# Performance work log

Measured on AMD Instinct MI355X. Metric: run time of the kernel, lower is better.

## Reference

```python
import jax, jax.numpy as jnp
import numpy as np

B, SZ_C, S, D_KV, H_DIM = 2048, 8, 32, 32, 512
NEG = B // 4  # batchsize > 64 branch
TEMP = 0.5
EPS = 1e-8
BN_EPS = 1e-5


def setup_inputs() -> dict:
    key = jax.random.key(0)
    ks = jax.random.split(key, 8)
    x = jax.random.normal(ks[0], (B, SZ_C, S, D_KV), dtype=jnp.float32)
    W1 = jax.random.normal(ks[1], (H_DIM, D_KV), dtype=jnp.float32) * 0.05
    b1 = jnp.zeros((H_DIM,), jnp.float32)
    gamma = jnp.ones((H_DIM,), jnp.float32)
    beta = jnp.zeros((H_DIM,), jnp.float32)
    W2 = jax.random.normal(ks[2], (D_KV, H_DIM), dtype=jnp.float32) * 0.05
    b2 = jnp.zeros((D_KV,), jnp.float32)
    fcW = jax.random.normal(ks[3], (32, S * D_KV), dtype=jnp.float32) * 0.03
    fcb = jnp.zeros((32,), jnp.float32)
    # negatives: raw draws in [0, B-1); shifted past the self index inside reference
    neg_idx = jax.random.randint(ks[4], (B, NEG), 0, B - 1, dtype=jnp.int32)
    return {"x": x, "W1": W1, "b1": b1, "gamma": gamma, "beta": beta,
            "W2": W2, "b2": b2, "fcW": fcW, "fcb": fcb, "neg_idx": neg_idx}


def reference(x, W1, b1, gamma, beta, W2, b2, fcW, fcb, neg_idx):
    # per-channel MLP with training-mode BatchNorm (stats over the B*S rows of each channel)
    xc = jnp.transpose(x, (1, 0, 2, 3)).reshape(SZ_C, B * S, D_KV)   # [C, N, d_kv]
    h = jnp.einsum('cnd,hd->cnh', xc, W1) + b1                        # [C, N, h]
    mu = jnp.mean(h, axis=1, keepdims=True)
    var = jnp.mean((h - mu) ** 2, axis=1, keepdims=True)              # biased, as BN
    h = jax.nn.relu((h - mu) * jax.lax.rsqrt(var + BN_EPS) * gamma + beta)
    y = jnp.einsum('cnh,dh->cnd', h, W2) + b2                         # [C, N, d_kv]
    y = y.reshape(SZ_C, B, S * D_KV)                                  # raw flatten == torch views
    Zc = jnp.einsum('cbf,of->cbo', y, fcW) + fcb                      # [C, B, 32]
    Z = jnp.transpose(Zc, (1, 0, 2))                                  # [B, C, 32]

    Zn = Z / jnp.clip(jnp.linalg.norm(Z, axis=-1, keepdims=True), EPS, None)

    # shift raw draws in [0, B-1) past i -> uniform over indices != i
    idx = neg_idx + (neg_idx >= jnp.arange(B, dtype=neg_idx.dtype)[:, None]).astype(neg_idx.dtype)
    neg = Zn[idx]                                                     # [B, NEG, C, 32]
    neg_sim = jnp.einsum('bcd,bncd->bn', Zn, neg) / SZ_C              # mean over channels

    # mean pairwise cosine similarity across channels (j < k)
    G = jnp.einsum('bjd,bkd->bjk', Zn, Zn)                            # [B, C, C]
    mask = jnp.triu(jnp.ones((SZ_C, SZ_C), bool), 1)
    num_comb = SZ_C * (SZ_C - 1) // 2
    pos_sim = jnp.where(mask, G, 0.0).sum(axis=(1, 2)) / num_comb     # [B]

    l = jnp.exp(pos_sim / TEMP) / jnp.sum(jnp.exp(neg_sim / TEMP), axis=1)  # [B]
    Z_out = jnp.mean(Z, axis=1)                                       # [B, 32]
    return Z_out, l
```

## Files before the change

kernel.cpp:

```cpp
#include <hip/hip_runtime.h>
#include <hip/hip_bf16.h>
#include <math.h>

#define NB 2048
#define NC 8
#define NNEG 512

typedef __attribute__((ext_vector_type(8))) short bf16x8;
typedef __attribute__((ext_vector_type(4))) float f32x4;
typedef __attribute__((ext_vector_type(16))) float f32x16;

static __device__ __forceinline__ unsigned short f2b(float f) {
  __hip_bfloat16 h = __float2bfloat16(f);
  return *reinterpret_cast<unsigned short*>(&h);
}
static __device__ __forceinline__ unsigned int pack_rn(float a, float b) {
  unsigned int ua = __float_as_uint(a) + 0x8000u;
  unsigned int ub = __float_as_uint(b) + 0x8000u;
  return __builtin_amdgcn_perm(ub, ua, 0x07060302u);
}
#define MF16(a, b, c) __builtin_amdgcn_mfma_f32_16x16x32_bf16((a), (b), (c), 0, 0, 0)

#define WS_SSUM   0
#define WS_SPROD  256
#define WS_B1EFF  8448
#define WS_Z      12544
#define WS_POS    536832
#define WS_W1B    538880
#define WS_W2B    604416
#define WS_FCWB   612608
#define WS_ZNB    628992

__global__ __launch_bounds__(256) void k_stats(const float* __restrict__ x,
                        float* __restrict__ Ssum, float* __restrict__ Sprod) {
  int c = blockIdx.y;
  int t = threadIdx.x;
  int w = t >> 6, l = t & 63;
  int col = l & 31, half = l >> 5;
  f32x16 acc;
  #pragma unroll
  for (int r = 0; r < 16; ++r) acc[r] = 0.f;
  float ssum = 0.f;
  #pragma unroll 2
  for (int i = 0; i < 8; ++i) {
    int chunk = blockIdx.x * 32 + i * 4 + w;
    int b = chunk >> 1;
    int sb = (chunk & 1) * 16 + half * 8;
    const float* base = x + ((size_t)(b * NC + c)) * 1024 + sb * 32 + col;
    float v0 = base[0],   v1 = base[32],  v2 = base[64],  v3 = base[96];
    float v4 = base[128], v5 = base[160], v6 = base[192], v7 = base[224];
    ssum += ((v0 + v1) + (v2 + v3)) + ((v4 + v5) + (v6 + v7));
    uint4 fq;
    fq.x = pack_rn(v0, v1); fq.y = pack_rn(v2, v3);
    fq.z = pack_rn(v4, v5); fq.w = pack_rn(v6, v7);
    bf16x8 f = __builtin_bit_cast(bf16x8, fq);
    acc = __builtin_amdgcn_mfma_f32_32x32x16_bf16(f, f, acc, 0, 0, 0);
  }
  __shared__ float pr[4][1024];
  __shared__ float sred[4][32];
  #pragma unroll
  for (int r = 0; r < 16; ++r) {
    int row = (r & 3) + 8 * (r >> 2) + 4 * half;
    pr[w][row * 32 + col] = acc[r];
  }
  float sv = ssum + __shfl_xor(ssum, 32);
  if (l < 32) sred[w][l] = sv;
  __syncthreads();
  #pragma unroll
  for (int p = 0; p < 4; ++p) {
    int cell = t + p * 256;
    atomicAdd(&Sprod[c * 1024 + cell],
              (pr[0][cell] + pr[1][cell]) + (pr[2][cell] + pr[3][cell]));
  }
  if (t < 32)
    atomicAdd(&Ssum[c * 32 + t],
              (sred[0][t] + sred[1][t]) + (sred[2][t] + sred[3][t]));
}

__global__ void k_foldcvt(const float* __restrict__ W1, const float* __restrict__ b1,
                       const float* __restrict__ gamma, const float* __restrict__ beta,
                       const float* __restrict__ Ssum, const float* __restrict__ Sprod,
                       const float* __restrict__ W2, const float* __restrict__ fcW,
                       unsigned short* __restrict__ W1B, float* __restrict__ b1eff,
                       unsigned short* __restrict__ W2B, unsigned short* __restrict__ fcWB) {
  if (blockIdx.x >= 16) {
    int j = (blockIdx.x - 16) * 256 + threadIdx.x;
    if (j < 8192)
      ((unsigned int*)W2B)[j] = pack_rn(W2[2 * j], W2[2 * j + 1]);
    ((unsigned int*)fcWB)[j] = pack_rn(fcW[2 * j], fcW[2 * j + 1]);
    return;
  }
  int g = blockIdx.x * 256 + threadIdx.x;
  int c = g >> 9, h = g & 511;
  const float invN = 1.0f / (float)(NB * 32);
  float w[32];
  #pragma unroll
  for (int d = 0; d < 32; ++d) w[d] = W1[h * 32 + d];
  const float* M = Sprod + c * 1024;
  float q = 0.f;
  for (int j = 0; j < 32; ++j) {
    float v = 0.f;
    #pragma unroll
    for (int i2 = 0; i2 < 32; ++i2) v = fmaf(w[i2], M[i2 * 32 + j], v);
    q = fmaf(v, w[j], q);
  }
  float wmu = 0.f;
  #pragma unroll
  for (int d = 0; d < 32; ++d) wmu = fmaf(w[d], Ssum[c * 32 + d] * invN, wmu);
  float bb = b1[h];
  float mean = wmu + bb;
  float e2 = q * invN + 2.f * bb * wmu + bb * bb;
  float var = e2 - mean * mean;
  float alpha = gamma[h] * rsqrtf(var + 1e-5f);
  unsigned int* W1Bu = (unsigned int*)&W1B[((size_t)c * 512 + h) * 32];
  #pragma unroll
  for (int d = 0; d < 16; ++d)
    W1Bu[d] = pack_rn(w[2 * d] * alpha, w[2 * d + 1] * alpha);
  b1eff[c * 512 + h] = (bb - mean) * alpha + beta[h];
}

__global__ __launch_bounds__(256, 2) void k_main(
    const float* __restrict__ x, const unsigned short* __restrict__ W1B,
    const float* __restrict__ b1eff, const unsigned short* __restrict__ W2B,
    const float* __restrict__ b2, const unsigned short* __restrict__ fcWB,
    const float* __restrict__ fcb, float* __restrict__ Z) {
  int c = blockIdx.y;
  int bt0 = blockIdx.x * 4;
  int t = threadIdx.x;
  int w = t >> 6, l = t & 63;
  int lr = l & 15, lg = l >> 4;

  __shared__ unsigned int rbuf[4][64][20];
  __shared__ float zred[2][8][32];

  const unsigned short* W1c = W1B + (size_t)c * 512 * 32;
  const float* b1e = b1eff + c * 512;
  unsigned int* rbw = &rbuf[w][0][0];

  bf16x8 wfR[2];   f32x4 biasR[2];   bf16x8 w2fR[2];   bf16x8 hfreg[4];
  bf16x8 xf[4], xfN[4];

#define LOADX(dst, bti) \
  _Pragma("unroll") for (int sb = 0; sb < 4; ++sb) { \
    int bl = 2 * w + (sb >> 1); \
    int s = (sb & 1) * 16 + lr; \
    const float* src = x + (((size_t)((bti) * 8 + bl) * NC + c) * 32 + s) * 32 + lg * 8; \
    float4 v0 = ((const float4*)src)[0]; \
    float4 v1 = ((const float4*)src)[1]; \
    uint4 fq; \
    fq.x = pack_rn(v0.x, v0.y); fq.y = pack_rn(v0.z, v0.w); \
    fq.z = pack_rn(v1.x, v1.y); fq.w = pack_rn(v1.z, v1.w); \
    dst[sb] = __builtin_bit_cast(bf16x8, fq); \
  }

#define LDWF0() { \
    wfR[0]  = *(const bf16x8*)&W1c[(size_t)lr * 32 + lg * 8]; \
    wfR[1]  = *(const bf16x8*)&W1c[(size_t)(16 + lr) * 32 + lg * 8]; \
    biasR[0] = *(const f32x4*)(b1e + lg * 4); \
    biasR[1] = *(const f32x4*)(b1e + 16 + lg * 4); }

#define GEMM1(dfr) \
  _Pragma("unroll") for (int hb = 0; hb < 2; ++hb) \
  _Pragma("unroll") for (int sb = 0; sb < 4; ++sb) \
    dfr[hb][sb] = MF16(wfR[hb], xf[sb], biasR[hb]);

#define GEMM2() \
  _Pragma("unroll") for (int mb = 0; mb < 4; ++mb) { \
    yacc[mb][0] = MF16(w2fR[0], hfreg[mb], yacc[mb][0]); \
    yacc[mb][1] = MF16(w2fR[1], hfreg[mb], yacc[mb][1]); \
  }

#define PACKWRITE(dfr) \
  _Pragma("unroll") for (int hb = 0; hb < 2; ++hb) \
  _Pragma("unroll") for (int sb = 0; sb < 4; ++sb) { \
    uint2 pk; \
    pk.x = pack_rn(fmaxf(dfr[hb][sb][0], 0.f), fmaxf(dfr[hb][sb][1], 0.f)); \
    pk.y = pack_rn(fmaxf(dfr[hb][sb][2], 0.f), fmaxf(dfr[hb][sb][3], 0.f)); \
    *(uint2*)&rbw[(sb * 16 + lr) * 20 + hb * 8 + lg * 2] = pk; \
  }

#define LOADW(ch) { \
    if ((ch) < 15) { \
      int h1 = ((ch) + 1) * 32; \
      wfR[0]  = *(const bf16x8*)&W1c[(size_t)(h1 + lr) * 32 + lg * 8]; \
      wfR[1]  = *(const bf16x8*)&W1c[(size_t)(h1 + 16 + lr) * 32 + lg * 8]; \
      biasR[0] = *(const f32x4*)(b1e + h1 + lg * 4); \
      biasR[1] = *(const f32x4*)(b1e + h1 + 16 + lg * 4); \
    } \
    w2fR[0] = *(const bf16x8*)&W2B[(size_t)lr * 512 + (ch) * 32 + lg * 8]; \
    w2fR[1] = *(const bf16x8*)&W2B[(size_t)(16 + lr) * 512 + (ch) * 32 + lg * 8]; \
  }

#define READH() \
  _Pragma("unroll") for (int mb = 0; mb < 4; ++mb) \
    hfreg[mb] = *(const bf16x8*)&rbw[(mb * 16 + lr) * 20 + lg * 4];

  LOADX(xf, bt0);
  LDWF0();

  for (int tt = 0; tt < 4; ++tt) {
    int bt = bt0 + tt;

    f32x4 yacc[4][2];
    #pragma unroll
    for (int db = 0; db < 2; ++db) {
      f32x4 bv = *((const f32x4*)(b2 + db * 16 + lg * 4));
      #pragma unroll
      for (int mb = 0; mb < 4; ++mb) yacc[mb][db] = bv;
    }

    {
      f32x4 dfr[2][4];
      GEMM1(dfr);
      PACKWRITE(dfr);
      LOADW(0);
      READH();
    }
    #pragma unroll 3
    for (int ch = 1; ch < 16; ++ch) {
      f32x4 dfr[2][4];
      GEMM1(dfr);
      GEMM2();
      PACKWRITE(dfr);
      LOADW(ch);
      READH();
    }
    GEMM2();

    if (tt < 3) LOADX(xfN, bt + 1);
    LDWF0();

    #pragma unroll
    for (int mb = 0; mb < 4; ++mb) {
      #pragma unroll
      for (int db = 0; db < 2; ++db) {
        uint2 pk;
        pk.x = pack_rn(yacc[mb][db][0], yacc[mb][db][1]);
        pk.y = pack_rn(yacc[mb][db][2], yacc[mb][db][3]);
        *(uint2*)&rbw[(mb * 16 + lr) * 20 + db * 8 + lg * 2] = pk;
      }
    }
    __syncthreads();

    {
      int nt = w & 1, kh = w >> 1;
      int arow = (lr < 8) ? lr : 7;
      const unsigned int* ybase = &rbuf[arow >> 1][(arow & 1) * 32][0];
      f32x4 zacc = {0.f, 0.f, 0.f, 0.f};
      #pragma unroll
      for (int ks = 0; ks < 16; ++ks) {
        int s = kh * 16 + ks;
        uint4 av = *(const uint4*)&ybase[s * 20 + lg * 4];
        bf16x8 afc = __builtin_bit_cast(bf16x8, av);
        bf16x8 bfc = *(const bf16x8*)&fcWB[(size_t)(nt * 16 + lr) * 1024 + s * 32 + lg * 8];
        zacc = MF16(afc, bfc, zacc);
      }
      if (lg < 2) {
        #pragma unroll
        for (int r = 0; r < 4; ++r) zred[kh][lg * 4 + r][nt * 16 + lr] = zacc[r];
      }
    }
    __syncthreads();
    {
      int bloc = t >> 5, o = t & 31;
      Z[((size_t)(bt * 8 + bloc) * NC + c) * 32 + o] =
          zred[0][bloc][o] + zred[1][bloc][o] + fcb[o];
    }
    if (tt < 3) {
      #pragma unroll
      for (int sb = 0; sb < 4; ++sb) xf[sb] = xfN[sb];
    }
  }
#undef LOADX
#undef LDWF0
#undef GEMM1
#undef GEMM2
#undef PACKWRITE
#undef LOADW
#undef READH
}

__global__ void k_znorm(const float* __restrict__ Z, unsigned short* __restrict__ Znb,
                        float* __restrict__ possim, float* __restrict__ out) {
  int b = blockIdx.x;
  int t = threadIdx.x;
  float v = Z[(size_t)b * 256 + t];
  float n2 = v * v;
  #pragma unroll
  for (int m = 16; m >= 1; m >>= 1) n2 += __shfl_xor(n2, m, 64);
  float nrm = fmaxf(sqrtf(n2), 1e-8f);
  float zn = v / nrm;
  Znb[(size_t)b * 256 + t] = f2b(zn);
  __shared__ float sz[256];
  __shared__ float szn[256];
  sz[t] = v; szn[t] = zn;
  __syncthreads();
  if (t < 32) {
    float s = 0.f;
    #pragma unroll
    for (int cc = 0; cc < 8; ++cc) s += sz[cc * 32 + t];
    out[(size_t)b * 32 + t] = s * 0.125f;
    float sd = 0.f, t1 = 0.f;
    #pragma unroll
    for (int cc = 0; cc < 8; ++cc) {
      float z2 = szn[cc * 32 + t];
      sd += z2; t1 = fmaf(z2, z2, t1);
    }
    float t2 = sd * sd;
    #pragma unroll
    for (int m = 16; m >= 1; m >>= 1) {
      t2 += __shfl_xor(t2, m, 64);
      t1 += __shfl_xor(t1, m, 64);
    }
    if (t == 0) possim[b] = (t2 - t1) * 0.5f / 28.0f;
  }
}

__global__ __launch_bounds__(256) void k_negsim(
    const unsigned short* __restrict__ Znb, const int* __restrict__ neg_idx,
    const float* __restrict__ possim, float* __restrict__ lout) {
  int b = blockIdx.x;
  int t = threadIdx.x;
  int w = t >> 6, l = t & 63;
  int lr = l & 15, lg = l >> 4;
  __shared__ uint4 selfv[32];
  __shared__ float rs[4];
  if (t < 32) selfv[t] = ((const uint4*)(Znb + (size_t)b * 256))[t];
  __syncthreads();
  const unsigned short* selfp = (const unsigned short*)selfv;
  const f32x4 fzero = {0.f, 0.f, 0.f, 0.f};
  float esum = 0.f;
  #pragma unroll 2
  for (int mb = 0; mb < 8; ++mb) {
    int m0 = w * 128 + mb * 16;
    int raw = neg_idx[(size_t)b * NNEG + m0 + lr];
    int j = raw + (raw >= b ? 1 : 0);
    const unsigned short* rp = Znb + (size_t)j * 256;
    f32x4 acc = fzero;
    #pragma unroll
    for (int ks = 0; ks < 8; ++ks) {
      bf16x8 af = *(const bf16x8*)(rp + ks * 32 + lg * 8);
      bf16x8 bf = *(const bf16x8*)(selfp + ks * 32 + lg * 8);
      acc = MF16(af, bf, acc);
    }
    if (lr == 0) {
      esum += expf(acc[0] * 0.25f) + expf(acc[1] * 0.25f)
            + expf(acc[2] * 0.25f) + expf(acc[3] * 0.25f);
    }
  }
  #pragma unroll
  for (int m = 32; m >= 1; m >>= 1) esum += __shfl_xor(esum, m, 64);
  if (l == 0) rs[w] = esum;
  __syncthreads();
  if (t == 0) {
    float tot = rs[0] + rs[1] + rs[2] + rs[3];
    lout[b] = expf(possim[b] * 2.0f) / tot;
  }
}

extern "C" void kernel_launch(void* const* d_in, const int* in_sizes, int n_in,
                              void* d_out, int out_size, void* d_ws, size_t ws_size,
                              hipStream_t stream) {
  const float* x     = (const float*)d_in[0];
  const float* W1    = (const float*)d_in[1];
  const float* b1    = (const float*)d_in[2];
  const float* gamma = (const float*)d_in[3];
  const float* beta  = (const float*)d_in[4];
  const float* W2    = (const float*)d_in[5];
  const float* b2    = (const float*)d_in[6];
  const float* fcW   = (const float*)d_in[7];
  const float* fcb   = (const float*)d_in[8];
  const int*   nidx  = (const int*)d_in[9];
  float* ws = (float*)d_ws;
  float* Ssum   = ws + WS_SSUM;
  float* Sprod  = ws + WS_SPROD;
  float* b1eff  = ws + WS_B1EFF;
  float* Z      = ws + WS_Z;
  float* possim = ws + WS_POS;
  unsigned short* W1Bp  = (unsigned short*)(ws + WS_W1B);
  unsigned short* W2Bp  = (unsigned short*)(ws + WS_W2B);
  unsigned short* fcWBp = (unsigned short*)(ws + WS_FCWB);
  unsigned short* Znbp  = (unsigned short*)(ws + WS_ZNB);
  float* out = (float*)d_out;

  hipMemsetAsync(ws, 0, (256 + 8192) * sizeof(float), stream);
  k_stats<<<dim3(128, 8), 256, 0, stream>>>(x, Ssum, Sprod);
  k_foldcvt<<<80, 256, 0, stream>>>(W1, b1, gamma, beta, Ssum, Sprod, W2, fcW,
                                    W1Bp, b1eff, W2Bp, fcWBp);
  k_main<<<dim3(64, 8), 256, 0, stream>>>(x, W1Bp, b1eff, W2Bp, b2, fcWBp, fcb, Z);
  k_znorm<<<NB, 256, 0, stream>>>(Z, Znbp, possim, out);
  k_negsim<<<NB, 256, 0, stream>>>(Znbp, nidx, possim, out + NB * 32);
}
```

Baseline: 176.9 us.

## Replace stats atomics with partial buffers and double-buffer the MLP hidden chunks

The stats kernel now writes per-block partial Gram and sum tiles to scratch instead of issuing global atomics. A new small reduction kernel sums them, which also drops the memset. The main kernel processes two hidden-dim chunks per iteration using A/B register sets and two LDS buffers, so GEMM1 of one chunk overlaps GEMM2 of the other. This raises register and LDS use and adds one kernel launch.

```diff
diff --git a/kernel.cpp b/kernel.cpp
--- a/kernel.cpp
+++ b/kernel.cpp
@@ -30,9 +30,10 @@
 #define WS_W2B    604416
 #define WS_FCWB   612608
 #define WS_ZNB    628992
+#define WS_SSUMP  891136
 
 __global__ __launch_bounds__(256) void k_stats(const float* __restrict__ x,
-                        float* __restrict__ Ssum, float* __restrict__ Sprod) {
+                        float* __restrict__ SsumP, float* __restrict__ SprodP) {
   int c = blockIdx.y;
   int t = threadIdx.x;
   int w = t >> 6, l = t & 63;
@@ -42,8 +43,8 @@
   for (int r = 0; r < 16; ++r) acc[r] = 0.f;
   float ssum = 0.f;
   #pragma unroll 2
-  for (int i = 0; i < 8; ++i) {
-    int chunk = blockIdx.x * 32 + i * 4 + w;
+  for (int i = 0; i < 16; ++i) {
+    int chunk = blockIdx.x * 64 + i * 4 + w;
     int b = chunk >> 1;
     int sb = (chunk & 1) * 16 + half * 8;
     const float* base = x + ((size_t)(b * NC + c)) * 1024 + sb * 32 + col;
@@ -69,12 +70,33 @@
   #pragma unroll
   for (int p = 0; p < 4; ++p) {
     int cell = t + p * 256;
-    atomicAdd(&Sprod[c * 1024 + cell],
-              (pr[0][cell] + pr[1][cell]) + (pr[2][cell] + pr[3][cell]));
+    SprodP[((size_t)(c * 64 + blockIdx.x)) * 1024 + cell] =
+        (pr[0][cell] + pr[1][cell]) + (pr[2][cell] + pr[3][cell]);
   }
   if (t < 32)
-    atomicAdd(&Ssum[c * 32 + t],
-              (sred[0][t] + sred[1][t]) + (sred[2][t] + sred[3][t]));
+    SsumP[(c * 64 + blockIdx.x) * 32 + t] =
+        (sred[0][t] + sred[1][t]) + (sred[2][t] + sred[3][t]);
+}
+
+__global__ void k_red(const float* __restrict__ SprodP, const float* __restrict__ SsumP,
+                      float* __restrict__ Sprod, float* __restrict__ Ssum) {
+  if (blockIdx.x < 32) {
+    int g = blockIdx.x * 256 + threadIdx.x;
+    int c = g >> 10, cell = g & 1023;
+    float s = 0.f;
+    #pragma unroll 8
+    for (int p = 0; p < 64; ++p)
+      s += SprodP[((size_t)(c * 64 + p)) * 1024 + cell];
+    Sprod[g] = s;
+  } else {
+    int t = threadIdx.x;
+    int c = t >> 5, d = t & 31;
+    float s = 0.f;
+    #pragma unroll 8
+    for (int p = 0; p < 64; ++p)
+      s += SsumP[(c * 64 + p) * 32 + d];
+    Ssum[t] = s;
+  }
 }
 
 __global__ void k_foldcvt(const float* __restrict__ W1, const float* __restrict__ b1,
@@ -130,14 +152,17 @@
   int w = t >> 6, l = t & 63;
   int lr = l & 15, lg = l >> 4;
 
-  __shared__ unsigned int rbuf[4][64][20];
+  __shared__ unsigned int rbuf[4][2][64][20];
   __shared__ float zred[2][8][32];
 
   const unsigned short* W1c = W1B + (size_t)c * 512 * 32;
   const float* b1e = b1eff + c * 512;
-  unsigned int* rbw = &rbuf[w][0][0];
-
-  bf16x8 wfR[2];   f32x4 biasR[2];   bf16x8 w2fR[2];   bf16x8 hfreg[4];
+  unsigned int* rbA = &rbuf[w][0][0][0];
+  unsigned int* rbB = &rbuf[w][1][0][0];
+
+  bf16x8 wfA[2], wfB[2];  f32x4 biA[2], biB[2];
+  bf16x8 w2A[2], w2B[2];
+  bf16x8 hfA[4], hfB[4];
   bf16x8 xf[4], xfN[4];
 
 #define LOADX(dst, bti) \
@@ -153,51 +178,45 @@
     dst[sb] = __builtin_bit_cast(bf16x8, fq); \
   }
 
-#define LDWF0() { \
-    wfR[0]  = *(const bf16x8*)&W1c[(size_t)lr * 32 + lg * 8]; \
-    wfR[1]  = *(const bf16x8*)&W1c[(size_t)(16 + lr) * 32 + lg * 8]; \
-    biasR[0] = *(const f32x4*)(b1e + lg * 4); \
-    biasR[1] = *(const f32x4*)(b1e + 16 + lg * 4); }
-
-#define GEMM1(dfr) \
+#define LDWF(WF, BI, ch) { int h1_ = (ch) * 32; \
+    WF[0] = *(const bf16x8*)&W1c[(size_t)(h1_ + lr) * 32 + lg * 8]; \
+    WF[1] = *(const bf16x8*)&W1c[(size_t)(h1_ + 16 + lr) * 32 + lg * 8]; \
+    BI[0] = *(const f32x4*)(b1e + h1_ + lg * 4); \
+    BI[1] = *(const f32x4*)(b1e + h1_ + 16 + lg * 4); }
+
+#define LDW2(WR, ch) { \
+    WR[0] = *(const bf16x8*)&W2B[(size_t)lr * 512 + (ch) * 32 + lg * 8]; \
+    WR[1] = *(const bf16x8*)&W2B[(size_t)(16 + lr) * 512 + (ch) * 32 + lg * 8]; }
+
+#define GEMM1(dfr, WF, BI) \
   _Pragma("unroll") for (int hb = 0; hb < 2; ++hb) \
   _Pragma("unroll") for (int sb = 0; sb < 4; ++sb) \
-    dfr[hb][sb] = MF16(wfR[hb], xf[sb], biasR[hb]);
-
-#define GEMM2() \
+    dfr[hb][sb] = MF16(WF[hb], xf[sb], BI[hb]);
+
+#define GEMM2(HF, WR) \
   _Pragma("unroll") for (int mb = 0; mb < 4; ++mb) { \
-    yacc[mb][0] = MF16(w2fR[0], hfreg[mb], yacc[mb][0]); \
-    yacc[mb][1] = MF16(w2fR[1], hfreg[mb], yacc[mb][1]); \
-  }
-
-#define PACKWRITE(dfr) \
+    yacc[mb][0] = MF16(WR[0], HF[mb], yacc[mb][0]); \
+    yacc[mb][1] = MF16(WR[1], HF[mb], yacc[mb][1]); \
+  }
+
+#define PACKW(dfr, RB) \
   _Pragma("unroll") for (int hb = 0; hb < 2; ++hb) \
   _Pragma("unroll") for (int sb = 0; sb < 4; ++sb) { \
     uint2 pk; \
     pk.x = pack_rn(fmaxf(dfr[hb][sb][0], 0.f), fmaxf(dfr[hb][sb][1], 0.f)); \
     pk.y = pack_rn(fmaxf(dfr[hb][sb][2], 0.f), fmaxf(dfr[hb][sb][3], 0.f)); \
-    *(uint2*)&rbw[(sb * 16 + lr) * 20 + hb * 8 + lg * 2] = pk; \
-  }
-
-#define LOADW(ch) { \
-    if ((ch) < 15) { \
-      int h1 = ((ch) + 1) * 32; \
-      wfR[0]  = *(const bf16x8*)&W1c[(size_t)(h1 + lr) * 32 + lg * 8]; \
-      wfR[1]  = *(const bf16x8*)&W1c[(size_t)(h1 + 16 + lr) * 32 + lg * 8]; \
-      biasR[0] = *(const f32x4*)(b1e + h1 + lg * 4); \
-      biasR[1] = *(const f32x4*)(b1e + h1 + 16 + lg * 4); \
-    } \
-    w2fR[0] = *(const bf16x8*)&W2B[(size_t)lr * 512 + (ch) * 32 + lg * 8]; \
-    w2fR[1] = *(const bf16x8*)&W2B[(size_t)(16 + lr) * 512 + (ch) * 32 + lg * 8]; \
-  }
-
-#define READH() \
+    *(uint2*)&RB[(sb * 16 + lr) * 20 + hb * 8 + lg * 2] = pk; \
+  }
+
+#define READH(HF, RB) \
   _Pragma("unroll") for (int mb = 0; mb < 4; ++mb) \
-    hfreg[mb] = *(const bf16x8*)&rbw[(mb * 16 + lr) * 20 + lg * 4];
+    HF[mb] = *(const bf16x8*)&RB[(mb * 16 + lr) * 20 + lg * 4];
 
   LOADX(xf, bt0);
-  LDWF0();
-
+  LDWF(wfA, biA, 0);
+  LDWF(wfB, biB, 1);
+
+  #pragma unroll 1
   for (int tt = 0; tt < 4; ++tt) {
     int bt = bt0 + tt;
 
@@ -211,24 +230,41 @@
 
     {
       f32x4 dfr[2][4];
-      GEMM1(dfr);
-      PACKWRITE(dfr);
-      LOADW(0);
-      READH();
-    }
-    #pragma unroll 3
-    for (int ch = 1; ch < 16; ++ch) {
+      GEMM1(dfr, wfA, biA);
+      PACKW(dfr, rbA);
+      GEMM1(dfr, wfB, biB);
+      PACKW(dfr, rbB);
+      LDWF(wfA, biA, 2);
+      LDWF(wfB, biB, 3);
+      LDW2(w2A, 0);
+      LDW2(w2B, 1);
+      READH(hfA, rbA);
+      READH(hfB, rbB);
+    }
+    for (int p = 1; p < 8; ++p) {
+      int a = 2 * p;
       f32x4 dfr[2][4];
-      GEMM1(dfr);
-      GEMM2();
-      PACKWRITE(dfr);
-      LOADW(ch);
-      READH();
-    }
-    GEMM2();
+      GEMM1(dfr, wfA, biA);
+      GEMM2(hfA, w2A);
+      PACKW(dfr, rbA);
+      GEMM1(dfr, wfB, biB);
+      GEMM2(hfB, w2B);
+      PACKW(dfr, rbB);
+      if (p < 7) {
+        LDWF(wfA, biA, a + 2);
+        LDWF(wfB, biB, a + 3);
+      }
+      LDW2(w2A, a);
+      LDW2(w2B, a + 1);
+      READH(hfA, rbA);
+      READH(hfB, rbB);
+    }
+    GEMM2(hfA, w2A);
+    GEMM2(hfB, w2B);
 
     if (tt < 3) LOADX(xfN, bt + 1);
-    LDWF0();
+    LDWF(wfA, biA, 0);
+    LDWF(wfB, biB, 1);
 
     #pragma unroll
     for (int mb = 0; mb < 4; ++mb) {
@@ -237,7 +273,7 @@
         uint2 pk;
         pk.x = pack_rn(yacc[mb][db][0], yacc[mb][db][1]);
         pk.y = pack_rn(yacc[mb][db][2], yacc[mb][db][3]);
-        *(uint2*)&rbw[(mb * 16 + lr) * 20 + db * 8 + lg * 2] = pk;
+        *(uint2*)&rbA[(mb * 16 + lr) * 20 + db * 8 + lg * 2] = pk;
       }
     }
     __syncthreads();
@@ -245,7 +281,7 @@
     {
       int nt = w & 1, kh = w >> 1;
       int arow = (lr < 8) ? lr : 7;
-      const unsigned int* ybase = &rbuf[arow >> 1][(arow & 1) * 32][0];
+      const unsigned int* ybase = &rbuf[arow >> 1][0][(arow & 1) * 32][0];
       f32x4 zacc = {0.f, 0.f, 0.f, 0.f};
       #pragma unroll
       for (int ks = 0; ks < 16; ++ks) {
@@ -272,11 +308,11 @@
     }
   }
 #undef LOADX
-#undef LDWF0
+#undef LDWF
+#undef LDW2
 #undef GEMM1
 #undef GEMM2
-#undef PACKWRITE
-#undef LOADW
+#undef PACKW
 #undef READH
 }
 
@@ -376,6 +412,8 @@
   float* Sprod  = ws + WS_SPROD;
   float* b1eff  = ws + WS_B1EFF;
   float* Z      = ws + WS_Z;
+  float* SprodP = ws + WS_Z;
+  float* SsumP  = ws + WS_SSUMP;
   float* possim = ws + WS_POS;
   unsigned short* W1Bp  = (unsigned short*)(ws + WS_W1B);
   unsigned short* W2Bp  = (unsigned short*)(ws + WS_W2B);
@@ -383,8 +421,8 @@
   unsigned short* Znbp  = (unsigned short*)(ws + WS_ZNB);
   float* out = (float*)d_out;
 
-  hipMemsetAsync(ws, 0, (256 + 8192) * sizeof(float), stream);
-  k_stats<<<dim3(128, 8), 256, 0, stream>>>(x, Ssum, Sprod);
+  k_stats<<<dim3(64, 8), 256, 0, stream>>>(x, SsumP, SprodP);
+  k_red<<<33, 256, 0, stream>>>(SprodP, SsumP, Sprod, Ssum);
   k_foldcvt<<<80, 256, 0, stream>>>(W1, b1, gamma, beta, Ssum, Sprod, W2, fcW,
                                     W1Bp, b1eff, W2Bp, fcWBp);
   k_main<<<dim3(64, 8), 256, 0, stream>>>(x, W1Bp, b1eff, W2Bp, b2, fcWBp, fcb, Z);
```

Result: slower. 195.8 us (+10.7%).
